# Kernel tuning notes

Hardware: AMD Instinct MI355X
Metric: run time of the kernel (lower is better)

The kernel has to match this reference:

```python
import jax, jax.numpy as jnp
import numpy as np
from jax import lax

B, C, IMG, PATCH = 128, 3, 224, 16
EMB, HEADS = 384, 6
NPATCH = (IMG // PATCH) ** 2          # 196
NTOK = NPATCH + 1                     # 197 (cls token)
HID = int(EMB * 4.0)                  # 1536 (also expert hidden)
NE, K = 4, 2                          # num_experts (hardcoded 4), top-k
NCLS = 1000


def _ln(x, g, b, eps=1e-5):
    m = jnp.mean(x, axis=-1, keepdims=True)
    v = jnp.mean((x - m) ** 2, axis=-1, keepdims=True)
    return (x - m) * lax.rsqrt(v + eps) * g + b


def setup_inputs() -> dict:
    key = jax.random.key(0)
    ks = jax.random.split(key, 16)
    s = 0.02
    return {
        "x": jax.random.normal(ks[0], (B, C, IMG, IMG), jnp.float32),
        "conv_w": jax.random.normal(ks[1], (EMB, C, PATCH, PATCH), jnp.float32) * s,
        "conv_b": jnp.zeros((EMB,), jnp.float32),
        "cls_token": jax.random.normal(ks[2], (1, 1, EMB), jnp.float32) * s,
        "pos_embed": jax.random.normal(ks[3], (1, NTOK, EMB), jnp.float32) * s,
        "ln1_g": jnp.ones((EMB,), jnp.float32),
        "ln1_b": jnp.zeros((EMB,), jnp.float32),
        "in_proj_w": jax.random.normal(ks[4], (3 * EMB, EMB), jnp.float32) * s,
        "in_proj_b": jnp.zeros((3 * EMB,), jnp.float32),
        "out_proj_w": jax.random.normal(ks[5], (EMB, EMB), jnp.float32) * s,
        "out_proj_b": jnp.zeros((EMB,), jnp.float32),
        "router_w": jax.random.normal(ks[6], (NE, EMB), jnp.float32) * s,
        "router_b": jnp.zeros((NE,), jnp.float32),
        "ew1": jax.random.normal(ks[7], (NE, EMB, HID), jnp.float32) * s,
        "eb1": jnp.zeros((NE, HID), jnp.float32),
        "ew2": jax.random.normal(ks[8], (NE, HID, EMB), jnp.float32) * s,
        "eb2": jnp.zeros((NE, EMB), jnp.float32),
        "ln2_g": jnp.ones((EMB,), jnp.float32),
        "ln2_b": jnp.zeros((EMB,), jnp.float32),
        "head_w": jax.random.normal(ks[9], (NCLS, EMB), jnp.float32) * s,
        "head_b": jnp.zeros((NCLS,), jnp.float32),
    }


def reference(x, conv_w, conv_b, cls_token, pos_embed,
              ln1_g, ln1_b, in_proj_w, in_proj_b, out_proj_w, out_proj_b,
              router_w, router_b, ew1, eb1, ew2, eb2,
              ln2_g, ln2_b, head_w, head_b):
    # ---- patch embedding: Conv2d(stride=kernel=patch) -> [B, N, E]
    h = lax.conv_general_dilated(x, conv_w, window_strides=(PATCH, PATCH),
                                 padding="VALID",
                                 dimension_numbers=("NCHW", "OIHW", "NCHW"))
    h = h + conv_b[None, :, None, None]
    h = h.reshape(B, EMB, NPATCH).transpose(0, 2, 1)          # [B, 196, E]
    h = jnp.concatenate([jnp.broadcast_to(cls_token, (B, 1, EMB)), h], axis=1)
    h = h + pos_embed                                         # [B, 197, E]

    # ---- SelfAttentionBlock (NOTE: no residual; same LN applied twice, as in source)
    hn = _ln(h, ln1_g, ln1_b)
    qkv = hn @ in_proj_w.T + in_proj_b                        # [B, N, 3E]
    q, k, v = jnp.split(qkv, 3, axis=-1)
    hd = EMB // HEADS
    q = q.reshape(B, NTOK, HEADS, hd)
    k = k.reshape(B, NTOK, HEADS, hd)
    v = v.reshape(B, NTOK, HEADS, hd)
    att = jnp.einsum("bqhd,bkhd->bhqk", q, k) / np.sqrt(hd).astype(np.float32)
    att = jax.nn.softmax(att, axis=-1)
    o = jnp.einsum("bhqk,bkhd->bqhd", att, v).reshape(B, NTOK, EMB)
    o = o @ out_proj_w.T + out_proj_b
    h = _ln(o, ln1_g, ln1_b)                                  # second LN, same params

    # ---- MoE: dense all-expert FFN + top-k gather + mean
    scores = jax.nn.softmax(h @ router_w.T + router_b, axis=-1)   # [B, N, NE]
    topk_vals, topk_idx = lax.top_k(scores, K)                    # [B, N, K]
    flat = h.reshape(B * NTOK, EMB)
    eh = jax.nn.gelu(jnp.einsum("te,neh->tnh", flat, ew1) + eb1, approximate=False)
    eo = jnp.einsum("tnh,nhe->tne", eh, ew2) + eb2                # [BN, NE, E]
    idx = topk_idx.reshape(B * NTOK, K, 1)
    sel = jnp.take_along_axis(eo, idx, axis=1)                    # [BN, K, E]
    h = sel.mean(axis=1).reshape(B, NTOK, EMB)

    # ---- final norm + classification head on cls token
    h = _ln(h, ln2_g, ln2_b)
    return h[:, 0] @ head_w.T + head_b                            # [B, NCLS]
```

## Files before the change

kernel.cpp:

```cpp
#include <hip/hip_runtime.h>
#include <cstdint>
#include <cstddef>

typedef _Float16 f16;
typedef _Float16 f16x8 __attribute__((ext_vector_type(8)));
typedef float    f32x4 __attribute__((ext_vector_type(4)));

constexpr int NTOKC  = 197;
constexpr int TTOK   = 128 * 197;
constexpr int EMB    = 384;
constexpr int HID    = 1536;

constexpr size_t OFF_CONVW  = 0;
constexpr size_t OFF_KVW    = 589824;
constexpr size_t OFF_EW1T   = 1179648;
constexpr size_t OFF_EW2T   = 5898240;
constexpr size_t OFF_OCLS   = 10616832;
constexpr size_t OFF_O2CLS  = 10813440;
constexpr size_t OFF_HCLS16 = 11010048;
constexpr size_t OFF_MASKW  = 11108352;
constexpr size_t OFF_EH     = 11110400;
constexpr size_t OFF_EO     = 12683264;
constexpr size_t OFF_H      = 13500416;
constexpr size_t OFF_XH     = 52232192;
constexpr size_t OFF_KV     = 71598080;
constexpr size_t OFF_AIM    = OFF_KV;
constexpr size_t OFF_HEADW16 = OFF_KV + (size_t)TTOK * 768 * 4;
constexpr size_t OFF_HFIN   = OFF_HEADW16 + 786432;
constexpr size_t WS_NEEDED  = OFF_HFIN + 98304;

__device__ __forceinline__ void gload16(const void* g, void* l) {
  __builtin_amdgcn_global_load_lds(
      (__attribute__((address_space(1))) void*)(void*)g,
      (__attribute__((address_space(3))) void*)l, 16, 0, 0);
}

__global__ __launch_bounds__(256) void cast_f16_k(
    const float* __restrict__ in, f16* __restrict__ o, int n) {
  int i = blockIdx.x * 256 + threadIdx.x;
  if (i < n) o[i] = (f16)in[i];
}

__global__ __launch_bounds__(256) void cast_pad_k(
    const float* __restrict__ in, f16* __restrict__ o) {
// ... 9 lines not shown
  __shared__ float tile[32][33];
  int e = blockIdx.z;
  const float* pin = in + (size_t)e * R * C;
  f16* pout = outp + (size_t)e * R * C;
  int c0 = blockIdx.x * 32, r0 = blockIdx.y * 32;
  int tx = threadIdx.x & 31, ty = threadIdx.x >> 5;
#pragma unroll
  for (int i = 0; i < 4; i++)
    tile[ty + 8 * i][tx] = pin[(size_t)(r0 + ty + 8 * i) * C + c0 + tx];
  __syncthreads();
#pragma unroll
  for (int i = 0; i < 4; i++)
    pout[(size_t)(c0 + ty + 8 * i) * R + r0 + tx] = (f16)tile[tx][ty + 8 * i];
}

__global__ void cls_init_k(const float* __restrict__ cls, const float* __restrict__ posw,
                           float* __restrict__ h0) {
  int b = blockIdx.x, c = threadIdx.x;
  h0[(size_t)b * NTOKC * EMB + c] = cls[c] + posw[c];
}

__global__ __launch_bounds__(256) void im2col_k(
    const float* __restrict__ img, f16* __restrict__ A) {
  __shared__ float tile[16 * 224];
  int py = blockIdx.x, cch = blockIdx.y, b = blockIdx.z;
  const float* src = img + ((size_t)(b * 3 + cch) * 224 + py * 16) * 224;
  for (int i = threadIdx.x; i < 16 * 224; i += 256) tile[i] = src[i];
  __syncthreads();
  if (threadIdx.x < 224) {
    int px = threadIdx.x >> 4, ky = threadIdx.x & 15;
    size_t outb = ((size_t)(b * 196 + py * 14 + px)) * 768 + cch * 256 + ky * 16;
    f16 hv[16] __attribute__((aligned(16)));
#pragma unroll
    for (int t = 0; t < 16; t++) hv[t] = (f16)tile[ky * 224 + px * 16 + t];
    ((uint4*)(A + outb))[0] = ((uint4*)hv)[0];
    ((uint4*)(A + outb))[1] = ((uint4*)hv)[1];
  }
}

template <int EMBED>
__global__ __launch_bounds__(256) void gemm16_k(
    const f16* __restrict__ A, const f16* __restrict__ B,
    const float* __restrict__ bias, const float* __restrict__ posw,
    float* __restrict__ Cout, int K, int N) {
  __shared__ f16 As[128 * 32];
  __shared__ f16 Bs[128 * 32];
  const int tid = threadIdx.x;
  const int lane = tid & 63;
  const int wave = tid >> 6;
  const int m0 = (int)blockIdx.y * 128;
  const int n0 = (int)blockIdx.x * 128;
  const int wm = (wave >> 1) * 64;
  const int wn = (wave & 1) * 64;
  const int fr = lane & 15;
  const int fq = lane >> 4;

  f32x4 acc[4][4];
#pragma unroll
  for (int i = 0; i < 4; i++)
#pragma unroll
    for (int j = 0; j < 4; j++) acc[i][j] = f32x4{0.f, 0.f, 0.f, 0.f};
// ... 21 lines not shown
    for (int i = 0; i < 4; i++)
#pragma unroll
      for (int j = 0; j < 4; j++)
        acc[i][j] = __builtin_amdgcn_mfma_f32_16x16x32_f16(af[i], bf[j], acc[i][j], 0, 0, 0);
    __syncthreads();
  }

#pragma unroll
  for (int i = 0; i < 4; i++)
#pragma unroll
    for (int j = 0; j < 4; j++)
#pragma unroll
      for (int rg = 0; rg < 4; rg++) {
        int gm = m0 + wm + i * 16 + fq * 4 + rg;
        int gn = n0 + wn + j * 16 + fr;
        float v = acc[i][j][rg] + bias[gn];
        if (EMBED) {
          int bb = gm / 196;
          int pp = gm - bb * 196;
          Cout[((size_t)bb * NTOKC + pp + 1) * EMB + gn] =
              v + posw[(size_t)(pp + 1) * EMB + gn];
        } else {
          Cout[(size_t)gm * N + gn] = v;
        }
      }
}

template <int GELU>
__global__ __launch_bounds__(256) void moe_gemm_k(
    const f16* __restrict__ A, size_t aestride,
    const f16* __restrict__ Bm, size_t bestride,
    const float* __restrict__ bias, int biasstride,
    f16* __restrict__ outh, float* __restrict__ outf, size_t ostride,
    int K, int N) {
  __shared__ f16 As[128 * 32];
  __shared__ f16 Bs[128 * 32];
  const int tid = threadIdx.x;
  const int lane = tid & 63;
  const int wave = tid >> 6;
  const int e = (int)blockIdx.y;
  const int n0 = (int)blockIdx.x * 128;
  const int wm = (wave >> 1) * 64;
  const int wn = (wave & 1) * 64;
  const int fr = lane & 15;
  const int fq = lane >> 4;
  A += (size_t)e * aestride;
  Bm += (size_t)e * bestride;
  bias += (size_t)e * biasstride;

  f32x4 acc[4][4];
#pragma unroll
  for (int i = 0; i < 4; i++)
#pragma unroll
    for (int j = 0; j < 4; j++) acc[i][j] = f32x4{0.f, 0.f, 0.f, 0.f};

  const int srow = wave * 32 + (lane >> 2);
  const int scol = (lane & 3) * 8;
  const f16* ag = A + (size_t)srow * K + scol;
  const f16* bg = Bm + (size_t)(n0 + srow) * K + scol;
  const size_t rstep = (size_t)16 * K;
  f16* la = As + wave * 32 * 32;
  f16* lb = Bs + wave * 32 * 32;

  for (int k0 = 0; k0 < K; k0 += 32) {
    gload16(ag, la);          gload16(ag + rstep, la + 16 * 32);
    gload16(bg, lb);          gload16(bg + rstep, lb + 16 * 32);
    ag += 32; bg += 32;
    __syncthreads();
    f16x8 af[4], bf[4];
#pragma unroll
    for (int i = 0; i < 4; i++) {
      af[i] = *(const f16x8*)&As[(wm + i * 16 + fr) * 32 + fq * 8];
      bf[i] = *(const f16x8*)&Bs[(wn + i * 16 + fr) * 32 + fq * 8];
    }
#pragma unroll
    for (int i = 0; i < 4; i++)
#pragma unroll
      for (int j = 0; j < 4; j++)
        acc[i][j] = __builtin_amdgcn_mfma_f32_16x16x32_f16(af[i], bf[j], acc[i][j], 0, 0, 0);
    __syncthreads();
  }

#pragma unroll
  for (int i = 0; i < 4; i++)
#pragma unroll
    for (int j = 0; j < 4; j++)
#pragma unroll
      for (int rg = 0; rg < 4; rg++) {
        int gm = wm + i * 16 + fq * 4 + rg;
        int gn = n0 + wn + j * 16 + fr;
        float v = acc[i][j][rg] + bias[gn];
        if (GELU) {
          float g = 0.5f * v * (1.0f + erff(v * 0.70710678118654752f));
          outh[(size_t)e * ostride + (size_t)gm * N + gn] = (f16)g;
        } else {
          outf[(size_t)e * ostride + (size_t)gm * N + gn] = v;
        }
      }
}

__global__ __launch_bounds__(256) void head_gemm_k(
    const f16* __restrict__ A, const f16* __restrict__ B,
    const float* __restrict__ hb, float* __restrict__ outp) {
  __shared__ f16 As[128 * 32];
  __shared__ f16 Bs[128 * 32];
  const int K = 384;
  const int tid = threadIdx.x;
  const int lane = tid & 63;
  const int wave = tid >> 6;
  const int n0 = (int)blockIdx.x * 128;
  const int wm = (wave >> 1) * 64;
  const int wn = (wave & 1) * 64;
  const int fr = lane & 15;
// ... 31 lines not shown
        acc[i][j] = __builtin_amdgcn_mfma_f32_16x16x32_f16(af[i], bf[j], acc[i][j], 0, 0, 0);
    __syncthreads();
  }

#pragma unroll
  for (int i = 0; i < 4; i++)
#pragma unroll
    for (int j = 0; j < 4; j++)
#pragma unroll
      for (int rg = 0; rg < 4; rg++) {
        int gm = wm + i * 16 + fq * 4 + rg;
        int gn = n0 + wn + j * 16 + fr;
        if (gn < 1000)
          outp[(size_t)gm * 1000 + gn] = acc[i][j][rg] + hb[gn];
      }
}

__global__ __launch_bounds__(256) void ln_k(
    const float* __restrict__ in, const float* __restrict__ g, const float* __restrict__ bb,
    f16* __restrict__ oh) {
  int wave = threadIdx.x >> 6, lane = threadIdx.x & 63;
  size_t row = (size_t)blockIdx.x * 4 + wave;
  const float* xp = in + row * EMB;
  float v[6];
  float s = 0.f, sq = 0.f;
#pragma unroll
  for (int i = 0; i < 6; i++) {
    v[i] = xp[lane + 64 * i];
    s += v[i];
    sq += v[i] * v[i];
  }
#pragma unroll
  for (int off = 32; off; off >>= 1) {
    s += __shfl_xor(s, off);
    sq += __shfl_xor(sq, off);
  }
  float m = s * (1.f / 384.f);
  float var = sq * (1.f / 384.f) - m * m;
  float rs = rsqrtf(var + 1e-5f);
#pragma unroll
  for (int i = 0; i < 6; i++) {
    int c = lane + 64 * i;
    oh[row * EMB + c] = (f16)((v[i] - m) * rs * g[c] + bb[c]);
  }
}

__global__ __launch_bounds__(256) void attn_cls_k(
    const float* __restrict__ Hbuf, const float* __restrict__ g, const float* __restrict__ bb,
    const float* __restrict__ Wq, const float* __restrict__ bq,
    const float* __restrict__ kv, float* __restrict__ ocls) {
  __shared__ float xs[EMB];
  __shared__ float qs[64];
  __shared__ float red[8];
  __shared__ float qpart[4][64];
  __shared__ float racc[64 * 64];
  __shared__ float rsum[64];
  const int h = blockIdx.x, b = blockIdx.y;
  const int tid = threadIdx.x;
  const int wave = tid >> 6, lane = tid & 63;

  const float* xp = Hbuf + (size_t)b * NTOKC * EMB;
  float v0 = xp[tid];
  float v1 = (tid < 128) ? xp[256 + tid] : 0.f;
  float s = v0 + v1, sq = v0 * v0 + v1 * v1;
#pragma unroll
  for (int off = 32; off; off >>= 1) {
    s += __shfl_xor(s, off);
    sq += __shfl_xor(sq, off);
  }
  if (lane == 0) { red[wave] = s; red[4 + wave] = sq; }
  __syncthreads();
  float S = red[0] + red[1] + red[2] + red[3];
  float SQ = red[4] + red[5] + red[6] + red[7];
  float m = S * (1.f / 384.f);
  float rs = rsqrtf(SQ * (1.f / 384.f) - m * m + 1e-5f);
  xs[tid] = (v0 - m) * rs * g[tid] + bb[tid];
  if (tid < 128) xs[256 + tid] = (v1 - m) * rs * g[256 + tid] + bb[256 + tid];
  __syncthreads();

  {
    int d = tid & 63, part = tid >> 6;
    const float4* w4 = (const float4*)(Wq + (size_t)(h * 64 + d) * EMB + part * 96);
    const float4* s4 = (const float4*)(xs + part * 96);
    float a = 0.f;
#pragma unroll
    for (int i = 0; i < 24; i++) {
      float4 xx = s4[i], ww = w4[i];
      a += xx.x * ww.x + xx.y * ww.y + xx.z * ww.z + xx.w * ww.w;
    }
    qpart[part][d] = a;
  }
  __syncthreads();
  if (tid < 64)
    qs[tid] = bq[h * 64 + tid] + qpart[0][tid] + qpart[1][tid] + qpart[2][tid] + qpart[3][tid];
  __syncthreads();

  const int r4 = lane >> 2, c = lane & 3;
  const int rowslot = wave * 16 + r4;
  float qv[16];
#pragma unroll
  for (int j = 0; j < 16; j++) qv[j] = qs[c * 16 + j];
  float acc[16];
#pragma unroll
  for (int j = 0; j < 16; j++) acc[j] = 0.f;
  float lsum = 0.f;

#pragma unroll
  for (int i = 0; i < 4; i++) {
    int row = rowslot + 64 * i;
    if (row < NTOKC) {
      const float4* kp = (const float4*)(kv + ((size_t)b * NTOKC + row) * 768 + h * 64 + c * 16);
      float4 k0 = kp[0], k1 = kp[1], k2 = kp[2], k3 = kp[3];
      float sc = qv[0] * k0.x + qv[1] * k0.y + qv[2] * k0.z + qv[3] * k0.w +
                 qv[4] * k1.x + qv[5] * k1.y + qv[6] * k1.z + qv[7] * k1.w +
                 qv[8] * k2.x + qv[9] * k2.y + qv[10] * k2.z + qv[11] * k2.w +
                 qv[12] * k3.x + qv[13] * k3.y + qv[14] * k3.z + qv[15] * k3.w;
      sc += __shfl_xor(sc, 1);
      sc += __shfl_xor(sc, 2);
      float p = __expf(sc * 0.125f);
      lsum += p;
      const float4* vp = (const float4*)(kv + ((size_t)b * NTOKC + row) * 768 + 384 + h * 64 + c * 16);
      float4 w0 = vp[0], w1 = vp[1], w2 = vp[2], w3 = vp[3];
      acc[0] += p * w0.x;  acc[1] += p * w0.y;  acc[2] += p * w0.z;  acc[3] += p * w0.w;
      acc[4] += p * w1.x;  acc[5] += p * w1.y;  acc[6] += p * w1.z;  acc[7] += p * w1.w;
      acc[8] += p * w2.x;  acc[9] += p * w2.y;  acc[10] += p * w2.z; acc[11] += p * w2.w;
      acc[12] += p * w3.x; acc[13] += p * w3.y; acc[14] += p * w3.z; acc[15] += p * w3.w;
    }
  }
#pragma unroll
  for (int j = 0; j < 16; j++) racc[rowslot * 64 + c * 16 + j] = acc[j];
  if (c == 0) rsum[rowslot] = lsum;
  __syncthreads();

  if (tid < 64) {
    float o = 0.f, ls = 0.f;
#pragma unroll 8
    for (int r = 0; r < 64; r++) {
      o += racc[r * 64 + tid];
      ls += rsum[r];
    }
    ocls[(size_t)b * EMB + h * 64 + tid] = o / ls;
  }
}

__global__ __launch_bounds__(384) void rowproj_k(
    const float* __restrict__ xf, const float* __restrict__ W,
    const float* __restrict__ bias, float* __restrict__ outp) {
  __shared__ float hx[EMB];
  int b = blockIdx.x, t = threadIdx.x;
  hx[t] = xf[(size_t)b * EMB + t];
  __syncthreads();
  const float4* w4 = (const float4*)(W + (size_t)t * EMB);
  const float4* s4 = (const float4*)hx;
  float a = bias[t];
#pragma unroll 8
  for (int i = 0; i < 96; i++) {
    float4 x = s4[i], w = w4[i];
    a += x.x * w.x + x.y * w.y + x.z * w.z + x.w * w.w;
  }
  outp[(size_t)b * EMB + t] = a;
}

__global__ __launch_bounds__(384) void ln_router_k(
    const float* __restrict__ o2cls, const float* __restrict__ g, const float* __restrict__ bb,
    const float* __restrict__ rw, const float* __restrict__ rb,
    f16* __restrict__ hcls16, float* __restrict__ maskw) {
  __shared__ float red[16];
  __shared__ float part[6][4];
  __shared__ float logits[4];
  int b = blockIdx.x, t = threadIdx.x;
  int lane = t & 63, wave = t >> 6;
  float v = o2cls[(size_t)b * EMB + t];
  float s = v, sq = v * v;
#pragma unroll
  for (int off = 32; off; off >>= 1) {
    s += __shfl_xor(s, off);
    sq += __shfl_xor(sq, off);
  }
  if (lane == 0) { red[wave] = s; red[8 + wave] = sq; }
  __syncthreads();
  float S = 0.f, SQ = 0.f;
#pragma unroll
  for (int i = 0; i < 6; i++) { S += red[i]; SQ += red[8 + i]; }
  float m = S * (1.f / 384.f);
  float rs = rsqrtf(SQ * (1.f / 384.f) - m * m + 1e-5f);
  float y = (v - m) * rs * g[t] + bb[t];
  hcls16[(size_t)b * EMB + t] = (f16)y;
  float p0 = y * rw[t];
  float p1 = y * rw[EMB + t];
  float p2 = y * rw[2 * EMB + t];
  float p3 = y * rw[3 * EMB + t];
#pragma unroll
  for (int off = 32; off; off >>= 1) {
    p0 += __shfl_xor(p0, off);
    p1 += __shfl_xor(p1, off);
    p2 += __shfl_xor(p2, off);
    p3 += __shfl_xor(p3, off);
  }
  if (lane == 0) { part[wave][0] = p0; part[wave][1] = p1; part[wave][2] = p2; part[wave][3] = p3; }
  __syncthreads();
  if (t < 4) {
    float a = rb[t];
#pragma unroll
    for (int i = 0; i < 6; i++) a += part[i][t];
    logits[t] = a;
  }
  __syncthreads();
  if (t == 0) {
    float l0 = logits[0], l1 = logits[1], l2 = logits[2], l3 = logits[3];
    int i1 = 0; float b1 = l0;
    if (l1 > b1) { b1 = l1; i1 = 1; }
    if (l2 > b1) { b1 = l2; i1 = 2; }
    if (l3 > b1) { b1 = l3; i1 = 3; }
    int i2 = -1; float b2 = 0.f;
    float lv[4] = {l0, l1, l2, l3};
#pragma unroll
    for (int i = 0; i < 4; i++) {
      if (i == i1) continue;
      if (i2 < 0 || lv[i] > b2) { i2 = i; b2 = lv[i]; }
    }
#pragma unroll
    for (int e = 0; e < 4; e++)
      maskw[(size_t)b * 4 + e] = (e == i1 || e == i2) ? 0.5f : 0.f;
  }
}

__global__ __launch_bounds__(384) void combine_ln2_k(
    const float* __restrict__ eo, const float* __restrict__ maskw,
    const float* __restrict__ g, const float* __restrict__ bb,
    f16* __restrict__ hfin) {
  __shared__ float red[16];
  int b = blockIdx.x, t = threadIdx.x;
  int lane = t & 63, wave = t >> 6;
  float mw0 = maskw[b * 4 + 0], mw1 = maskw[b * 4 + 1];
  float mw2 = maskw[b * 4 + 2], mw3 = maskw[b * 4 + 3];
  const size_t eb = (size_t)b * EMB;
  const size_t es = (size_t)128 * EMB;
  float v = mw0 * eo[eb + t] + mw1 * eo[es + eb + t] +
            mw2 * eo[2 * es + eb + t] + mw3 * eo[3 * es + eb + t];
  float s = v, sq = v * v;
#pragma unroll
  for (int off = 32; off; off >>= 1) {
    s += __shfl_xor(s, off);
    sq += __shfl_xor(sq, off);
  }
  if (lane == 0) { red[wave] = s; red[8 + wave] = sq; }
  __syncthreads();
  float S = 0.f, SQ = 0.f;
#pragma unroll
  for (int i = 0; i < 6; i++) { S += red[i]; SQ += red[8 + i]; }
  float m = S * (1.f / 384.f);
  float rs = rsqrtf(SQ * (1.f / 384.f) - m * m + 1e-5f);
  hfin[(size_t)b * EMB + t] = (f16)((v - m) * rs * g[t] + bb[t]);
}

extern "C" void kernel_launch(void* const* d_in, const int* in_sizes, int n_in,
                              void* d_out, int out_size, void* d_ws, size_t ws_size,
                              hipStream_t stream) {
  const float* x      = (const float*)d_in[0];
  const float* conv_w = (const float*)d_in[1];
  const float* conv_b = (const float*)d_in[2];
  const float* cls_t  = (const float*)d_in[3];
  const float* pos    = (const float*)d_in[4];
  const float* ln1_g  = (const float*)d_in[5];
  const float* ln1_b  = (const float*)d_in[6];
  const float* inp_w  = (const float*)d_in[7];
  const float* inp_b  = (const float*)d_in[8];
  const float* outp_w = (const float*)d_in[9];
// ... 4 lines not shown
  const float* eb1    = (const float*)d_in[14];
  const float* ew2    = (const float*)d_in[15];
  const float* eb2    = (const float*)d_in[16];
  const float* ln2_g  = (const float*)d_in[17];
  const float* ln2_b  = (const float*)d_in[18];
  const float* head_w = (const float*)d_in[19];
  const float* head_b = (const float*)d_in[20];
  float* out = (float*)d_out;
  char* w = (char*)d_ws;
  if (ws_size < WS_NEEDED) return;

  f16* convw    = (f16*)(w + OFF_CONVW);
  f16* kvw      = (f16*)(w + OFF_KVW);
  f16* ew1t     = (f16*)(w + OFF_EW1T);
  f16* ew2t     = (f16*)(w + OFF_EW2T);
  float* ocls   = (float*)(w + OFF_OCLS);
  float* o2cls  = (float*)(w + OFF_O2CLS);
  f16* hcls16   = (f16*)(w + OFF_HCLS16);
  float* maskw  = (float*)(w + OFF_MASKW);
  f16* ehbuf    = (f16*)(w + OFF_EH);
  float* eobuf  = (float*)(w + OFF_EO);
  float* Hbuf   = (float*)(w + OFF_H);
  f16* xh       = (f16*)(w + OFF_XH);
  float* kvbuf  = (float*)(w + OFF_KV);
  f16* aim      = (f16*)(w + OFF_AIM);
  f16* headw16  = (f16*)(w + OFF_HEADW16);
  f16* hfin     = (f16*)(w + OFF_HFIN);

  cast_f16_k<<<dim3((294912 + 255) / 256), 256, 0, stream>>>(conv_w, convw, 294912);
  cast_f16_k<<<dim3((294912 + 255) / 256), 256, 0, stream>>>(inp_w + 384 * 384, kvw, 294912);
  cast_pad_k<<<dim3((1024 * 384 + 255) / 256), 256, 0, stream>>>(head_w, headw16);
  transpose_cast_k<<<dim3(48, 12, 4), 256, 0, stream>>>(ew1, ew1t, 384, 1536);
  transpose_cast_k<<<dim3(12, 48, 4), 256, 0, stream>>>(ew2, ew2t, 1536, 384);

  im2col_k<<<dim3(14, 3, 128), 256, 0, stream>>>(x, aim);
  gemm16_k<1><<<dim3(3, 196), 256, 0, stream>>>(aim, convw, conv_b, pos, Hbuf, 768, EMB);
  cls_init_k<<<dim3(128), dim3(384), 0, stream>>>(cls_t, pos, Hbuf);

  ln_k<<<dim3(TTOK / 4), 256, 0, stream>>>(Hbuf, ln1_g, ln1_b, xh);

  gemm16_k<0><<<dim3(6, 197), 256, 0, stream>>>(xh, kvw, inp_b + 384, nullptr, kvbuf, EMB, 768);

  attn_cls_k<<<dim3(6, 128), 256, 0, stream>>>(
      Hbuf, ln1_g, ln1_b, inp_w, inp_b, kvbuf, ocls);

  rowproj_k<<<dim3(128), 384, 0, stream>>>(ocls, outp_w, outp_b, o2cls);

  ln_router_k<<<dim3(128), 384, 0, stream>>>(
      o2cls, ln1_g, ln1_b, rt_w, rt_b, hcls16, maskw);

  moe_gemm_k<1><<<dim3(12, 4), 256, 0, stream>>>(
      hcls16, 0, ew1t, (size_t)HID * EMB, eb1, HID,
      ehbuf, nullptr, (size_t)128 * HID, EMB, HID);
  moe_gemm_k<0><<<dim3(3, 4), 256, 0, stream>>>(
      ehbuf, (size_t)128 * HID, ew2t, (size_t)EMB * HID, eb2, EMB,
      nullptr, eobuf, (size_t)128 * EMB, HID, EMB);

  combine_ln2_k<<<dim3(128), 384, 0, stream>>>(eobuf, maskw, ln2_g, ln2_b, hfin);
  head_gemm_k<<<dim3(8), 256, 0, stream>>>(hfin, headw16, head_b, out);
  (void)in_sizes; (void)n_in; (void)out_size;
}
```

Before: 394.5 us.

## Fuse patch-embed GEMM with LayerNorm, store K/V in fp16, split-K the MoE GEMMs

Replaces the patch-embedding GEMM plus separate LayerNorm pass with one kernel. It computes full 384-wide rows per block and applies bias, positional embedding and LN in registers, writing fp16 activations directly. This removes the fp32 H buffer round trip. The cls-token LN and Q projection are computed once in a single block and broadcast, since the cls input is the same across the batch. K/V are stored as fp16 to halve attention read traffic. The MoE GEMMs get smaller N tiles and split-K partials to raise block counts, at the cost of an extra partial-sum reduction in the combine kernel and reduced KV precision.

```diff
diff --git a/kernel.cpp b/kernel.cpp
--- a/kernel.cpp
+++ b/kernel.cpp
@@ -11,23 +11,24 @@
 constexpr int EMB    = 384;
 constexpr int HID    = 1536;
 
-constexpr size_t OFF_CONVW  = 0;
-constexpr size_t OFF_KVW    = 589824;
-constexpr size_t OFF_EW1T   = 1179648;
-constexpr size_t OFF_EW2T   = 5898240;
-constexpr size_t OFF_OCLS   = 10616832;
-constexpr size_t OFF_O2CLS  = 10813440;
-constexpr size_t OFF_HCLS16 = 11010048;
-constexpr size_t OFF_MASKW  = 11108352;
-constexpr size_t OFF_EH     = 11110400;
-constexpr size_t OFF_EO     = 12683264;
-constexpr size_t OFF_H      = 13500416;
-constexpr size_t OFF_XH     = 52232192;
-constexpr size_t OFF_KV     = 71598080;
-constexpr size_t OFF_AIM    = OFF_KV;
-constexpr size_t OFF_HEADW16 = OFF_KV + (size_t)TTOK * 768 * 4;
-constexpr size_t OFF_HFIN   = OFF_HEADW16 + 786432;
-constexpr size_t WS_NEEDED  = OFF_HFIN + 98304;
+constexpr size_t OFF_CONVW   = 0;
+constexpr size_t OFF_KVW     = 589824;
+constexpr size_t OFF_EW1T    = 1179648;
+constexpr size_t OFF_EW2T    = 5898240;
+constexpr size_t OFF_HEADW16 = 10616832;
+constexpr size_t OFF_XCLS16  = 11403264;
+constexpr size_t OFF_Q       = 11404800;
+constexpr size_t OFF_OCLS    = 11406336;
+constexpr size_t OFF_O2CLS   = 11602944;
+constexpr size_t OFF_HCLS16  = 11799552;
+constexpr size_t OFF_MASKW   = 11897856;
+constexpr size_t OFF_EH      = 11899904;
+constexpr size_t OFF_EPART   = 13472768;
+constexpr size_t OFF_HFIN    = 16618496;
+constexpr size_t OFF_XH      = 16716800;
+constexpr size_t OFF_KV      = 36082688;
+constexpr size_t OFF_AIM     = 74814464;
+constexpr size_t WS_NEEDED   = 113349632;
 
 __device__ __forceinline__ void gload16(const void* g, void* l) {
   __builtin_amdgcn_global_load_lds(
@@ -67,10 +68,47 @@
     pout[(size_t)(c0 + ty + 8 * i) * R + r0 + tx] = (f16)tile[tx][ty + 8 * i];
 }
 
-__global__ void cls_init_k(const float* __restrict__ cls, const float* __restrict__ posw,
-                           float* __restrict__ h0) {
-  int b = blockIdx.x, c = threadIdx.x;
-  h0[(size_t)b * NTOKC * EMB + c] = cls[c] + posw[c];
+__global__ __launch_bounds__(384) void clsprep_k(
+    const float* __restrict__ cls, const float* __restrict__ posw,
+    const float* __restrict__ g, const float* __restrict__ bb,
+    const float* __restrict__ Wq, const float* __restrict__ bq,
+    f16* __restrict__ xcls16, float* __restrict__ qout) {
+  __shared__ float xs[EMB];
+  __shared__ float red[16];
+  int t = threadIdx.x, lane = t & 63, wave = t >> 6;
+  float v = cls[t] + posw[t];
+  float s = v, sq = v * v;
+#pragma unroll
+  for (int off = 32; off; off >>= 1) {
+    s += __shfl_xor(s, off);
+    sq += __shfl_xor(sq, off);
+  }
+  if (lane == 0) { red[wave] = s; red[8 + wave] = sq; }
+  __syncthreads();
+  float S = 0.f, SQ = 0.f;
+#pragma unroll
+  for (int i = 0; i < 6; i++) { S += red[i]; SQ += red[8 + i]; }
+  float m = S * (1.f / 384.f);
+  float rs = rsqrtf(SQ * (1.f / 384.f) - m * m + 1e-5f);
+  float y = (v - m) * rs * g[t] + bb[t];
+  xs[t] = y;
+  xcls16[t] = (f16)y;
+  __syncthreads();
+  const float4* w4 = (const float4*)(Wq + (size_t)t * EMB);
+  const float4* s4 = (const float4*)xs;
+  float a = bq[t];
+#pragma unroll 8
+  for (int i = 0; i < 96; i++) {
+    float4 xx = s4[i], ww = w4[i];
+    a += xx.x * ww.x + xx.y * ww.y + xx.z * ww.z + xx.w * ww.w;
+  }
+  qout[t] = a;
+}
+
+__global__ __launch_bounds__(384) void bcast_cls_k(
+    const f16* __restrict__ xcls16, f16* __restrict__ xh) {
+  int b = blockIdx.x, t = threadIdx.x;
+  xh[(size_t)b * NTOKC * EMB + t] = xcls16[t];
 }
 
 __global__ __launch_bounds__(256) void im2col_k(
@@ -91,13 +129,92 @@
   }
 }
 
-template <int EMBED>
-__global__ __launch_bounds__(256) void gemm16_k(
+__global__ __launch_bounds__(256) void embed_ln_k(
     const f16* __restrict__ A, const f16* __restrict__ B,
     const float* __restrict__ bias, const float* __restrict__ posw,
-    float* __restrict__ Cout, int K, int N) {
+    const float* __restrict__ g, const float* __restrict__ bb,
+    f16* __restrict__ xh) {
+  __shared__ f16 As[64 * 32];
+  __shared__ f16 Bs[384 * 32];
+  const int K = 768;
+  const int tid = threadIdx.x;
+  const int lane = tid & 63;
+  const int wave = tid >> 6;
+  const int m0 = (int)blockIdx.x * 64;
+  const int fr = lane & 15;
+  const int fq = lane >> 4;
+
+  f32x4 acc[24];
+#pragma unroll
+  for (int j = 0; j < 24; j++) acc[j] = f32x4{0.f, 0.f, 0.f, 0.f};
+
+  const int sr = lane >> 2;
+  const int sc = (lane & 3) * 8;
+  const f16* ag = A + (size_t)(m0 + wave * 16 + sr) * K + sc;
+  f16* la = As + wave * 16 * 32;
+  const f16* bg = B + (size_t)(wave * 96 + sr) * K + sc;
+  f16* lb = Bs + wave * 96 * 32;
+
+  for (int k0 = 0; k0 < K; k0 += 32) {
+    gload16(ag + k0, la);
+#pragma unroll
+    for (int t = 0; t < 6; t++)
+      gload16(bg + (size_t)(t * 16) * K + k0, lb + t * 16 * 32);
+    __syncthreads();
+    f16x8 af = *(const f16x8*)&As[(wave * 16 + fr) * 32 + fq * 8];
+#pragma unroll
+    for (int j = 0; j < 24; j++) {
+      f16x8 bf = *(const f16x8*)&Bs[(j * 16 + fr) * 32 + fq * 8];
+      acc[j] = __builtin_amdgcn_mfma_f32_16x16x32_f16(af, bf, acc[j], 0, 0, 0);
+    }
+    __syncthreads();
+  }
+
+  float* sCB = (float*)Bs;
+  float* sG  = sCB + 384;
+  float* sB2 = sG + 384;
+  for (int i = tid; i < 384; i += 256) {
+    sCB[i] = bias[i]; sG[i] = g[i]; sB2[i] = bb[i];
+  }
+  __syncthreads();
+
+#pragma unroll
+  for (int rg = 0; rg < 4; rg++) {
+    int row = m0 + wave * 16 + fq * 4 + rg;
+    int bimg = row / 196;
+    int pp = row - bimg * 196;
+    const float* prow = posw + (size_t)(pp + 1) * EMB;
+    float v[24];
+    float s = 0.f, sq = 0.f;
+#pragma unroll
+    for (int j = 0; j < 24; j++) {
+      int col = j * 16 + fr;
+      float t = acc[j][rg] + sCB[col] + prow[col];
+      v[j] = t;
+      s += t; sq += t * t;
+    }
+#pragma unroll
+    for (int off = 1; off < 16; off <<= 1) {
+      s += __shfl_xor(s, off);
+      sq += __shfl_xor(sq, off);
+    }
+    float m = s * (1.f / 384.f);
+    float rs = rsqrtf(sq * (1.f / 384.f) - m * m + 1e-5f);
+    f16* orow = xh + ((size_t)bimg * NTOKC + pp + 1) * EMB;
+#pragma unroll
+    for (int j = 0; j < 24; j++) {
+      int col = j * 16 + fr;
+      orow[col] = (f16)((v[j] - m) * rs * sG[col] + sB2[col]);
+    }
+  }
+}
+
+__global__ __launch_bounds__(256) void gemm_kv_k(
+    const f16* __restrict__ A, const f16* __restrict__ B,
+    const float* __restrict__ bias, f16* __restrict__ Cout) {
   __shared__ f16 As[128 * 32];
   __shared__ f16 Bs[128 * 32];
+  const int K = EMB, N = 768;
   const int tid = threadIdx.x;
   const int lane = tid & 63;
   const int wave = tid >> 6;
@@ -149,69 +266,200 @@
       for (int rg = 0; rg < 4; rg++) {
         int gm = m0 + wm + i * 16 + fq * 4 + rg;
         int gn = n0 + wn + j * 16 + fr;
-        float v = acc[i][j][rg] + bias[gn];
-        if (EMBED) {
-          int bb = gm / 196;
-          int pp = gm - bb * 196;
-          Cout[((size_t)bb * NTOKC + pp + 1) * EMB + gn] =
-              v + posw[(size_t)(pp + 1) * EMB + gn];
-        } else {
-          Cout[(size_t)gm * N + gn] = v;
-        }
+        Cout[(size_t)gm * N + gn] = (f16)(acc[i][j][rg] + bias[gn]);
       }
 }
 
-template <int GELU>
-__global__ __launch_bounds__(256) void moe_gemm_k(
-    const f16* __restrict__ A, size_t aestride,
-    const f16* __restrict__ Bm, size_t bestride,
-    const float* __restrict__ bias, int biasstride,
-    f16* __restrict__ outh, float* __restrict__ outf, size_t ostride,
-    int K, int N) {
+__global__ __launch_bounds__(256) void attn_cls_k(
+    const float* __restrict__ qg, const f16* __restrict__ kv,
+    float* __restrict__ ocls) {
+  __shared__ float racc[64 * 64];
+  __shared__ float rsum[64];
+  const int h = blockIdx.x, b = blockIdx.y;
+  const int tid = threadIdx.x;
+  const int wave = tid >> 6, lane = tid & 63;
+  const int r4 = lane >> 2, c = lane & 3;
+  const int rowslot = wave * 16 + r4;
+
+  float qv[16];
+#pragma unroll
+  for (int j = 0; j < 16; j++) qv[j] = qg[h * 64 + c * 16 + j];
+  float acc[16];
+#pragma unroll
+  for (int j = 0; j < 16; j++) acc[j] = 0.f;
+  float lsum = 0.f;
+
+#pragma unroll
+  for (int i = 0; i < 4; i++) {
+    int row = rowslot + 64 * i;
+    if (row < NTOKC) {
+      const f16* kp = kv + ((size_t)b * NTOKC + row) * 768 + h * 64 + c * 16;
+      f16x8 k0 = *(const f16x8*)kp;
+      f16x8 k1 = *(const f16x8*)(kp + 8);
+      float sc = 0.f;
+#pragma unroll
+      for (int j = 0; j < 8; j++) sc += qv[j] * (float)k0[j];
+#pragma unroll
+      for (int j = 0; j < 8; j++) sc += qv[8 + j] * (float)k1[j];
+      sc += __shfl_xor(sc, 1);
+      sc += __shfl_xor(sc, 2);
+      float p = __expf(sc * 0.125f);
+      lsum += p;
+      const f16* vp = kp + 384;
+      f16x8 v0 = *(const f16x8*)vp;
+      f16x8 v1 = *(const f16x8*)(vp + 8);
+#pragma unroll
+      for (int j = 0; j < 8; j++) acc[j] += p * (float)v0[j];
+#pragma unroll
+      for (int j = 0; j < 8; j++) acc[8 + j] += p * (float)v1[j];
+    }
+  }
+#pragma unroll
+  for (int j = 0; j < 16; j++) racc[rowslot * 64 + c * 16 + j] = acc[j];
+  if (c == 0) rsum[rowslot] = lsum;
+  __syncthreads();
+
+  if (tid < 64) {
+    float o = 0.f, ls = 0.f;
+#pragma unroll 8
+    for (int r = 0; r < 64; r++) {
+      o += racc[r * 64 + tid];
+      ls += rsum[r];
+    }
+    ocls[(size_t)b * EMB + h * 64 + tid] = o / ls;
+  }
+}
+
+__global__ __launch_bounds__(384) void rowproj_k(
+    const float* __restrict__ xf, const float* __restrict__ W,
+    const float* __restrict__ bias, float* __restrict__ outp) {
+  __shared__ float hx[EMB];
+  int b = blockIdx.x, t = threadIdx.x;
+  hx[t] = xf[(size_t)b * EMB + t];
+  __syncthreads();
+  const float4* w4 = (const float4*)(W + (size_t)t * EMB);
+  const float4* s4 = (const float4*)hx;
+  float a = bias[t];
+#pragma unroll 8
+  for (int i = 0; i < 96; i++) {
+    float4 x = s4[i], w = w4[i];
+    a += x.x * w.x + x.y * w.y + x.z * w.z + x.w * w.w;
+  }
+  outp[(size_t)b * EMB + t] = a;
+}
+
+__global__ __launch_bounds__(384) void ln_router_k(
+    const float* __restrict__ o2cls, const float* __restrict__ g, const float* __restrict__ bb,
+    const float* __restrict__ rw, const float* __restrict__ rb,
+    f16* __restrict__ hcls16, float* __restrict__ maskw) {
+  __shared__ float red[16];
+  __shared__ float part[6][4];
+  __shared__ float logits[4];
+  int b = blockIdx.x, t = threadIdx.x;
+  int lane = t & 63, wave = t >> 6;
+  float v = o2cls[(size_t)b * EMB + t];
+  float s = v, sq = v * v;
+#pragma unroll
+  for (int off = 32; off; off >>= 1) {
+    s += __shfl_xor(s, off);
+    sq += __shfl_xor(sq, off);
+  }
+  if (lane == 0) { red[wave] = s; red[8 + wave] = sq; }
+  __syncthreads();
+  float S = 0.f, SQ = 0.f;
+#pragma unroll
+  for (int i = 0; i < 6; i++) { S += red[i]; SQ += red[8 + i]; }
+  float m = S * (1.f / 384.f);
+  float rs = rsqrtf(SQ * (1.f / 384.f) - m * m + 1e-5f);
+  float y = (v - m) * rs * g[t] + bb[t];
+  hcls16[(size_t)b * EMB + t] = (f16)y;
+  float p0 = y * rw[t];
+  float p1 = y * rw[EMB + t];
+  float p2 = y * rw[2 * EMB + t];
+  float p3 = y * rw[3 * EMB + t];
+#pragma unroll
+  for (int off = 32; off; off >>= 1) {
+    p0 += __shfl_xor(p0, off);
+    p1 += __shfl_xor(p1, off);
+    p2 += __shfl_xor(p2, off);
+    p3 += __shfl_xor(p3, off);
+  }
+  if (lane == 0) { part[wave][0] = p0; part[wave][1] = p1; part[wave][2] = p2; part[wave][3] = p3; }
+  __syncthreads();
+  if (t < 4) {
+    float a = rb[t];
+#pragma unroll
+    for (int i = 0; i < 6; i++) a += part[i][t];
+    logits[t] = a;
+  }
+  __syncthreads();
+  if (t == 0) {
+    float l0 = logits[0], l1 = logits[1], l2 = logits[2], l3 = logits[3];
+    int i1 = 0; float b1 = l0;
+    if (l1 > b1) { b1 = l1; i1 = 1; }
+    if (l2 > b1) { b1 = l2; i1 = 2; }
+    if (l3 > b1) { b1 = l3; i1 = 3; }
+    int i2 = -1; float b2 = 0.f;
+    float lv[4] = {l0, l1, l2, l3};
+#pragma unroll
+    for (int i = 0; i < 4; i++) {
+      if (i == i1) continue;
+      if (i2 < 0 || lv[i] > b2) { i2 = i; b2 = lv[i]; }
+    }
+#pragma unroll
+    for (int e = 0; e < 4; e++)
+      maskw[(size_t)b * 4 + e] = (e == i1 || e == i2) ? 0.5f : 0.f;
+  }
+}
+
+__global__ __launch_bounds__(256) void moe1_k(
+    const f16* __restrict__ A, const f16* __restrict__ Bm,
+    const float* __restrict__ bias, f16* __restrict__ outh) {
   __shared__ f16 As[128 * 32];
-  __shared__ f16 Bs[128 * 32];
+  __shared__ f16 Bs[64 * 32];
+  const int K = EMB;
   const int tid = threadIdx.x;
   const int lane = tid & 63;
   const int wave = tid >> 6;
   const int e = (int)blockIdx.y;
-  const int n0 = (int)blockIdx.x * 128;
+  const int n0 = (int)blockIdx.x * 64;
   const int wm = (wave >> 1) * 64;
-  const int wn = (wave & 1) * 64;
+  const int wn = (wave & 1) * 32;
   const int fr = lane & 15;
   const int fq = lane >> 4;
-  A += (size_t)e * aestride;
-  Bm += (size_t)e * bestride;
-  bias += (size_t)e * biasstride;
-
-  f32x4 acc[4][4];
-#pragma unroll
-  for (int i = 0; i < 4; i++)
-#pragma unroll
-    for (int j = 0; j < 4; j++) acc[i][j] = f32x4{0.f, 0.f, 0.f, 0.f};
-
-  const int srow = wave * 32 + (lane >> 2);
-  const int scol = (lane & 3) * 8;
-  const f16* ag = A + (size_t)srow * K + scol;
-  const f16* bg = Bm + (size_t)(n0 + srow) * K + scol;
+  Bm += (size_t)e * HID * EMB;
+  bias += (size_t)e * HID;
+
+  f32x4 acc[4][2];
+#pragma unroll
+  for (int i = 0; i < 4; i++)
+#pragma unroll
+    for (int j = 0; j < 2; j++) acc[i][j] = f32x4{0.f, 0.f, 0.f, 0.f};
+
+  const int sr = lane >> 2;
+  const int sc = (lane & 3) * 8;
+  const f16* ag = A + (size_t)(wave * 32 + sr) * K + sc;
+  const f16* bg = Bm + (size_t)(n0 + wave * 16 + sr) * K + sc;
   const size_t rstep = (size_t)16 * K;
   f16* la = As + wave * 32 * 32;
-  f16* lb = Bs + wave * 32 * 32;
+  f16* lb = Bs + wave * 16 * 32;
 
   for (int k0 = 0; k0 < K; k0 += 32) {
-    gload16(ag, la);          gload16(ag + rstep, la + 16 * 32);
-    gload16(bg, lb);          gload16(bg + rstep, lb + 16 * 32);
+    gload16(ag, la);  gload16(ag + rstep, la + 16 * 32);
+    gload16(bg, lb);
     ag += 32; bg += 32;
     __syncthreads();
-    f16x8 af[4], bf[4];
-#pragma unroll
-    for (int i = 0; i < 4; i++) {
+    f16x8 af[4], bf[2];
+#pragma unroll
+    for (int i = 0; i < 4; i++)
       af[i] = *(const f16x8*)&As[(wm + i * 16 + fr) * 32 + fq * 8];
-      bf[i] = *(const f16x8*)&Bs[(wn + i * 16 + fr) * 32 + fq * 8];
-    }
+#pragma unroll
+    for (int j = 0; j < 2; j++)
+      bf[j] = *(const f16x8*)&Bs[(wn + j * 16 + fr) * 32 + fq * 8];
 #pragma unroll
     for (int i = 0; i < 4; i++)
 #pragma unroll
-      for (int j = 0; j < 4; j++)
+      for (int j = 0; j < 2; j++)
         acc[i][j] = __builtin_amdgcn_mfma_f32_16x16x32_f16(af[i], bf[j], acc[i][j], 0, 0, 0);
     __syncthreads();
   }
@@ -219,19 +467,112 @@
 #pragma unroll
   for (int i = 0; i < 4; i++)
 #pragma unroll
-    for (int j = 0; j < 4; j++)
+    for (int j = 0; j < 2; j++)
 #pragma unroll
       for (int rg = 0; rg < 4; rg++) {
         int gm = wm + i * 16 + fq * 4 + rg;
         int gn = n0 + wn + j * 16 + fr;
         float v = acc[i][j][rg] + bias[gn];
-        if (GELU) {
-          float g = 0.5f * v * (1.0f + erff(v * 0.70710678118654752f));
-          outh[(size_t)e * ostride + (size_t)gm * N + gn] = (f16)g;
-        } else {
-          outf[(size_t)e * ostride + (size_t)gm * N + gn] = v;
-        }
+        float gl = 0.5f * v * (1.0f + erff(v * 0.70710678118654752f));
+        outh[(size_t)e * 128 * HID + (size_t)gm * HID + gn] = (f16)gl;
       }
+}
+
+__global__ __launch_bounds__(256) void moe2_k(
+    const f16* __restrict__ EH, const f16* __restrict__ W2,
+    float* __restrict__ part) {
+  __shared__ f16 As[128 * 32];
+  __shared__ f16 Bs[64 * 32];
+  const int tid = threadIdx.x;
+  const int lane = tid & 63;
+  const int wave = tid >> 6;
+  const int n0 = (int)blockIdx.x * 64;
+  const int e = (int)blockIdx.y;
+  const int kc = (int)blockIdx.z;
+  const int wm = (wave >> 1) * 64;
+  const int wn = (wave & 1) * 32;
+  const int fr = lane & 15;
+  const int fq = lane >> 4;
+  const f16* A = EH + (size_t)e * 128 * HID + kc * 384;
+  const f16* B = W2 + (size_t)e * EMB * HID + kc * 384;
+
+  f32x4 acc[4][2];
+#pragma unroll
+  for (int i = 0; i < 4; i++)
+#pragma unroll
+    for (int j = 0; j < 2; j++) acc[i][j] = f32x4{0.f, 0.f, 0.f, 0.f};
+
+  const int sr = lane >> 2;
+  const int sc = (lane & 3) * 8;
+  const f16* ag = A + (size_t)(wave * 32 + sr) * HID + sc;
+  const f16* bg = B + (size_t)(n0 + wave * 16 + sr) * HID + sc;
+  const size_t rstep = (size_t)16 * HID;
+  f16* la = As + wave * 32 * 32;
+  f16* lb = Bs + wave * 16 * 32;
+
+  for (int k0 = 0; k0 < 384; k0 += 32) {
+    gload16(ag, la);  gload16(ag + rstep, la + 16 * 32);
+    gload16(bg, lb);
+    ag += 32; bg += 32;
+    __syncthreads();
+    f16x8 af[4], bf[2];
+#pragma unroll
+    for (int i = 0; i < 4; i++)
+      af[i] = *(const f16x8*)&As[(wm + i * 16 + fr) * 32 + fq * 8];
+#pragma unroll
+    for (int j = 0; j < 2; j++)
+      bf[j] = *(const f16x8*)&Bs[(wn + j * 16 + fr) * 32 + fq * 8];
+#pragma unroll
+    for (int i = 0; i < 4; i++)
+#pragma unroll
+      for (int j = 0; j < 2; j++)
+        acc[i][j] = __builtin_amdgcn_mfma_f32_16x16x32_f16(af[i], bf[j], acc[i][j], 0, 0, 0);
+    __syncthreads();
+  }
+
+#pragma unroll
+  for (int i = 0; i < 4; i++)
+#pragma unroll
+    for (int j = 0; j < 2; j++)
+#pragma unroll
+      for (int rg = 0; rg < 4; rg++) {
+        int gm = wm + i * 16 + fq * 4 + rg;
+        int gn = n0 + wn + j * 16 + fr;
+        part[(((size_t)kc * 4 + e) * 128 + gm) * EMB + gn] = acc[i][j][rg];
+      }
+}
+
+__global__ __launch_bounds__(384) void combine_ln2_k(
+    const float* __restrict__ part, const float* __restrict__ eb2,
+    const float* __restrict__ maskw,
+    const float* __restrict__ g, const float* __restrict__ bb,
+    f16* __restrict__ hfin) {
+  __shared__ float red[16];
+  int b = blockIdx.x, t = threadIdx.x;
+  int lane = t & 63, wave = t >> 6;
+  float v = 0.f;
+#pragma unroll
+  for (int e = 0; e < 4; e++) {
+    float s = eb2[e * EMB + t];
+#pragma unroll
+    for (int kc = 0; kc < 4; kc++)
+      s += part[(((size_t)kc * 4 + e) * 128 + b) * EMB + t];
+    v += maskw[b * 4 + e] * s;
+  }
+  float s = v, sq = v * v;
+#pragma unroll
+  for (int off = 32; off; off >>= 1) {
+    s += __shfl_xor(s, off);
+    sq += __shfl_xor(sq, off);
+  }
+  if (lane == 0) { red[wave] = s; red[8 + wave] = sq; }
+  __syncthreads();
+  float S = 0.f, SQ = 0.f;
+#pragma unroll
+  for (int i = 0; i < 6; i++) { S += red[i]; SQ += red[8 + i]; }
+  float m = S * (1.f / 384.f);
+  float rs = rsqrtf(SQ * (1.f / 384.f) - m * m + 1e-5f);
+  hfin[(size_t)b * EMB + t] = (f16)((v - m) * rs * g[t] + bb[t]);
 }
 
 __global__ __launch_bounds__(256) void head_gemm_k(
@@ -293,244 +634,6 @@
         if (gn < 1000)
           outp[(size_t)gm * 1000 + gn] = acc[i][j][rg] + hb[gn];
       }
-}
-
-__global__ __launch_bounds__(256) void ln_k(
-    const float* __restrict__ in, const float* __restrict__ g, const float* __restrict__ bb,
-    f16* __restrict__ oh) {
-  int wave = threadIdx.x >> 6, lane = threadIdx.x & 63;
-  size_t row = (size_t)blockIdx.x * 4 + wave;
-  const float* xp = in + row * EMB;
-  float v[6];
-  float s = 0.f, sq = 0.f;
-#pragma unroll
-  for (int i = 0; i < 6; i++) {
-    v[i] = xp[lane + 64 * i];
-    s += v[i];
-    sq += v[i] * v[i];
-  }
-#pragma unroll
-  for (int off = 32; off; off >>= 1) {
-    s += __shfl_xor(s, off);
-    sq += __shfl_xor(sq, off);
-  }
-  float m = s * (1.f / 384.f);
-  float var = sq * (1.f / 384.f) - m * m;
-  float rs = rsqrtf(var + 1e-5f);
-#pragma unroll
-  for (int i = 0; i < 6; i++) {
-    int c = lane + 64 * i;
-    oh[row * EMB + c] = (f16)((v[i] - m) * rs * g[c] + bb[c]);
-  }
-}
-
-__global__ __launch_bounds__(256) void attn_cls_k(
-    const float* __restrict__ Hbuf, const float* __restrict__ g, const float* __restrict__ bb,
-    const float* __restrict__ Wq, const float* __restrict__ bq,
-    const float* __restrict__ kv, float* __restrict__ ocls) {
-  __shared__ float xs[EMB];
-  __shared__ float qs[64];
-  __shared__ float red[8];
-  __shared__ float qpart[4][64];
-  __shared__ float racc[64 * 64];
-  __shared__ float rsum[64];
-  const int h = blockIdx.x, b = blockIdx.y;
-  const int tid = threadIdx.x;
-  const int wave = tid >> 6, lane = tid & 63;
-
-  const float* xp = Hbuf + (size_t)b * NTOKC * EMB;
-  float v0 = xp[tid];
-  float v1 = (tid < 128) ? xp[256 + tid] : 0.f;
-  float s = v0 + v1, sq = v0 * v0 + v1 * v1;
-#pragma unroll
-  for (int off = 32; off; off >>= 1) {
-    s += __shfl_xor(s, off);
-    sq += __shfl_xor(sq, off);
-  }
-  if (lane == 0) { red[wave] = s; red[4 + wave] = sq; }
-  __syncthreads();
-  float S = red[0] + red[1] + red[2] + red[3];
-  float SQ = red[4] + red[5] + red[6] + red[7];
-  float m = S * (1.f / 384.f);
-  float rs = rsqrtf(SQ * (1.f / 384.f) - m * m + 1e-5f);
-  xs[tid] = (v0 - m) * rs * g[tid] + bb[tid];
-  if (tid < 128) xs[256 + tid] = (v1 - m) * rs * g[256 + tid] + bb[256 + tid];
-  __syncthreads();
-
-  {
-    int d = tid & 63, part = tid >> 6;
-    const float4* w4 = (const float4*)(Wq + (size_t)(h * 64 + d) * EMB + part * 96);
-    const float4* s4 = (const float4*)(xs + part * 96);
-    float a = 0.f;
-#pragma unroll
-    for (int i = 0; i < 24; i++) {
-      float4 xx = s4[i], ww = w4[i];
-      a += xx.x * ww.x + xx.y * ww.y + xx.z * ww.z + xx.w * ww.w;
-    }
-    qpart[part][d] = a;
-  }
-  __syncthreads();
-  if (tid < 64)
-    qs[tid] = bq[h * 64 + tid] + qpart[0][tid] + qpart[1][tid] + qpart[2][tid] + qpart[3][tid];
-  __syncthreads();
-
-  const int r4 = lane >> 2, c = lane & 3;
-  const int rowslot = wave * 16 + r4;
-  float qv[16];
-#pragma unroll
-  for (int j = 0; j < 16; j++) qv[j] = qs[c * 16 + j];
-  float acc[16];
-#pragma unroll
-  for (int j = 0; j < 16; j++) acc[j] = 0.f;
-  float lsum = 0.f;
-
-#pragma unroll
-  for (int i = 0; i < 4; i++) {
-    int row = rowslot + 64 * i;
-    if (row < NTOKC) {
-      const float4* kp = (const float4*)(kv + ((size_t)b * NTOKC + row) * 768 + h * 64 + c * 16);
-      float4 k0 = kp[0], k1 = kp[1], k2 = kp[2], k3 = kp[3];
-      float sc = qv[0] * k0.x + qv[1] * k0.y + qv[2] * k0.z + qv[3] * k0.w +
-                 qv[4] * k1.x + qv[5] * k1.y + qv[6] * k1.z + qv[7] * k1.w +
-                 qv[8] * k2.x + qv[9] * k2.y + qv[10] * k2.z + qv[11] * k2.w +
-                 qv[12] * k3.x + qv[13] * k3.y + qv[14] * k3.z + qv[15] * k3.w;
-      sc += __shfl_xor(sc, 1);
-      sc += __shfl_xor(sc, 2);
-      float p = __expf(sc * 0.125f);
-      lsum += p;
-      const float4* vp = (const float4*)(kv + ((size_t)b * NTOKC + row) * 768 + 384 + h * 64 + c * 16);
-      float4 w0 = vp[0], w1 = vp[1], w2 = vp[2], w3 = vp[3];
-      acc[0] += p * w0.x;  acc[1] += p * w0.y;  acc[2] += p * w0.z;  acc[3] += p * w0.w;
-      acc[4] += p * w1.x;  acc[5] += p * w1.y;  acc[6] += p * w1.z;  acc[7] += p * w1.w;
-      acc[8] += p * w2.x;  acc[9] += p * w2.y;  acc[10] += p * w2.z; acc[11] += p * w2.w;
-      acc[12] += p * w3.x; acc[13] += p * w3.y; acc[14] += p * w3.z; acc[15] += p * w3.w;
-    }
-  }
-#pragma unroll
-  for (int j = 0; j < 16; j++) racc[rowslot * 64 + c * 16 + j] = acc[j];
-  if (c == 0) rsum[rowslot] = lsum;
-  __syncthreads();
-
-  if (tid < 64) {
-    float o = 0.f, ls = 0.f;
-#pragma unroll 8
-    for (int r = 0; r < 64; r++) {
-      o += racc[r * 64 + tid];
-      ls += rsum[r];
-    }
-    ocls[(size_t)b * EMB + h * 64 + tid] = o / ls;
-  }
-}
-
-__global__ __launch_bounds__(384) void rowproj_k(
-    const float* __restrict__ xf, const float* __restrict__ W,
-    const float* __restrict__ bias, float* __restrict__ outp) {
-  __shared__ float hx[EMB];
-  int b = blockIdx.x, t = threadIdx.x;
-  hx[t] = xf[(size_t)b * EMB + t];
-  __syncthreads();
-  const float4* w4 = (const float4*)(W + (size_t)t * EMB);
-  const float4* s4 = (const float4*)hx;
-  float a = bias[t];
-#pragma unroll 8
-  for (int i = 0; i < 96; i++) {
-    float4 x = s4[i], w = w4[i];
-    a += x.x * w.x + x.y * w.y + x.z * w.z + x.w * w.w;
-  }
-  outp[(size_t)b * EMB + t] = a;
-}
-
-__global__ __launch_bounds__(384) void ln_router_k(
-    const float* __restrict__ o2cls, const float* __restrict__ g, const float* __restrict__ bb,
-    const float* __restrict__ rw, const float* __restrict__ rb,
-    f16* __restrict__ hcls16, float* __restrict__ maskw) {
-  __shared__ float red[16];
-  __shared__ float part[6][4];
-  __shared__ float logits[4];
-  int b = blockIdx.x, t = threadIdx.x;
-  int lane = t & 63, wave = t >> 6;
-  float v = o2cls[(size_t)b * EMB + t];
-  float s = v, sq = v * v;
-#pragma unroll
-  for (int off = 32; off; off >>= 1) {
-    s += __shfl_xor(s, off);
-    sq += __shfl_xor(sq, off);
-  }
-  if (lane == 0) { red[wave] = s; red[8 + wave] = sq; }
-  __syncthreads();
-  float S = 0.f, SQ = 0.f;
-#pragma unroll
-  for (int i = 0; i < 6; i++) { S += red[i]; SQ += red[8 + i]; }
-  float m = S * (1.f / 384.f);
-  float rs = rsqrtf(SQ * (1.f / 384.f) - m * m + 1e-5f);
-  float y = (v - m) * rs * g[t] + bb[t];
-  hcls16[(size_t)b * EMB + t] = (f16)y;
-  float p0 = y * rw[t];
-  float p1 = y * rw[EMB + t];
-  float p2 = y * rw[2 * EMB + t];
-  float p3 = y * rw[3 * EMB + t];
-#pragma unroll
-  for (int off = 32; off; off >>= 1) {
-    p0 += __shfl_xor(p0, off);
-    p1 += __shfl_xor(p1, off);
-    p2 += __shfl_xor(p2, off);
-    p3 += __shfl_xor(p3, off);
-  }
-  if (lane == 0) { part[wave][0] = p0; part[wave][1] = p1; part[wave][2] = p2; part[wave][3] = p3; }
-  __syncthreads();
-  if (t < 4) {
-    float a = rb[t];
-#pragma unroll
-    for (int i = 0; i < 6; i++) a += part[i][t];
-    logits[t] = a;
-  }
-  __syncthreads();
-  if (t == 0) {
-    float l0 = logits[0], l1 = logits[1], l2 = logits[2], l3 = logits[3];
-    int i1 = 0; float b1 = l0;
-    if (l1 > b1) { b1 = l1; i1 = 1; }
-    if (l2 > b1) { b1 = l2; i1 = 2; }
-    if (l3 > b1) { b1 = l3; i1 = 3; }
-    int i2 = -1; float b2 = 0.f;
-    float lv[4] = {l0, l1, l2, l3};
-#pragma unroll
-    for (int i = 0; i < 4; i++) {
-      if (i == i1) continue;
-      if (i2 < 0 || lv[i] > b2) { i2 = i; b2 = lv[i]; }
-    }
-#pragma unroll
-    for (int e = 0; e < 4; e++)
-      maskw[(size_t)b * 4 + e] = (e == i1 || e == i2) ? 0.5f : 0.f;
-  }
-}
-
-__global__ __launch_bounds__(384) void combine_ln2_k(
-    const float* __restrict__ eo, const float* __restrict__ maskw,
-    const float* __restrict__ g, const float* __restrict__ bb,
-    f16* __restrict__ hfin) {
-  __shared__ float red[16];
-  int b = blockIdx.x, t = threadIdx.x;
-  int lane = t & 63, wave = t >> 6;
-  float mw0 = maskw[b * 4 + 0], mw1 = maskw[b * 4 + 1];
-  float mw2 = maskw[b * 4 + 2], mw3 = maskw[b * 4 + 3];
-  const size_t eb = (size_t)b * EMB;
-  const size_t es = (size_t)128 * EMB;
-  float v = mw0 * eo[eb + t] + mw1 * eo[es + eb + t] +
-            mw2 * eo[2 * es + eb + t] + mw3 * eo[3 * es + eb + t];
-  float s = v, sq = v * v;
-#pragma unroll
-  for (int off = 32; off; off >>= 1) {
-    s += __shfl_xor(s, off);
-    sq += __shfl_xor(sq, off);
-  }
-  if (lane == 0) { red[wave] = s; red[8 + wave] = sq; }
-  __syncthreads();
-  float S = 0.f, SQ = 0.f;
-#pragma unroll
-  for (int i = 0; i < 6; i++) { S += red[i]; SQ += red[8 + i]; }
-  float m = S * (1.f / 384.f);
-  float rs = rsqrtf(SQ * (1.f / 384.f) - m * m + 1e-5f);
-  hfin[(size_t)b * EMB + t] = (f16)((v - m) * rs * g[t] + bb[t]);
 }
 
 extern "C" void kernel_launch(void* const* d_in, const int* in_sizes, int n_in,
@@ -565,18 +668,19 @@
   f16* kvw      = (f16*)(w + OFF_KVW);
   f16* ew1t     = (f16*)(w + OFF_EW1T);
   f16* ew2t     = (f16*)(w + OFF_EW2T);
+  f16* headw16  = (f16*)(w + OFF_HEADW16);
+  f16* xcls16   = (f16*)(w + OFF_XCLS16);
+  float* qvec   = (float*)(w + OFF_Q);
   float* ocls   = (float*)(w + OFF_OCLS);
   float* o2cls  = (float*)(w + OFF_O2CLS);
   f16* hcls16   = (f16*)(w + OFF_HCLS16);
   float* maskw  = (float*)(w + OFF_MASKW);
   f16* ehbuf    = (f16*)(w + OFF_EH);
-  float* eobuf  = (float*)(w + OFF_EO);
-  float* Hbuf   = (float*)(w + OFF_H);
+  float* epart  = (float*)(w + OFF_EPART);
+  f16* hfin     = (f16*)(w + OFF_HFIN);
   f16* xh       = (f16*)(w + OFF_XH);
-  float* kvbuf  = (float*)(w + OFF_KV);
+  f16* kvbuf    = (f16*)(w + OFF_KV);
   f16* aim      = (f16*)(w + OFF_AIM);
-  f16* headw16  = (f16*)(w + OFF_HEADW16);
-  f16* hfin     = (f16*)(w + OFF_HFIN);
 
   cast_f16_k<<<dim3((294912 + 255) / 256), 256, 0, stream>>>(conv_w, convw, 294912);
   cast_f16_k<<<dim3((294912 + 255) / 256), 256, 0, stream>>>(inp_w + 384 * 384, kvw, 294912);
@@ -584,30 +688,25 @@
   transpose_cast_k<<<dim3(48, 12, 4), 256, 0, stream>>>(ew1, ew1t, 384, 1536);
   transpose_cast_k<<<dim3(12, 48, 4), 256, 0, stream>>>(ew2, ew2t, 1536, 384);
 
+  clsprep_k<<<dim3(1), 384, 0, stream>>>(cls_t, pos, ln1_g, ln1_b, inp_w, inp_b, xcls16, qvec);
+  bcast_cls_k<<<dim3(128), 384, 0, stream>>>(xcls16, xh);
+
   im2col_k<<<dim3(14, 3, 128), 256, 0, stream>>>(x, aim);
-  gemm16_k<1><<<dim3(3, 196), 256, 0, stream>>>(aim, convw, conv_b, pos, Hbuf, 768, EMB);
-  cls_init_k<<<dim3(128), dim3(384), 0, stream>>>(cls_t, pos, Hbuf);
-
-  ln_k<<<dim3(TTOK / 4), 256, 0, stream>>>(Hbuf, ln1_g, ln1_b, xh);
-
-  gemm16_k<0><<<dim3(6, 197), 256, 0, stream>>>(xh, kvw, inp_b + 384, nullptr, kvbuf, EMB, 768);
-
-  attn_cls_k<<<dim3(6, 128), 256, 0, stream>>>(
-      Hbuf, ln1_g, ln1_b, inp_w, inp_b, kvbuf, ocls);
+  embed_ln_k<<<dim3(392), 256, 0, stream>>>(aim, convw, conv_b, pos, ln1_g, ln1_b, xh);
+
+  gemm_kv_k<<<dim3(6, 197), 256, 0, stream>>>(xh, kvw, inp_b + 384, kvbuf);
+
+  attn_cls_k<<<dim3(6, 128), 256, 0, stream>>>(qvec, kvbuf, ocls);
 
   rowproj_k<<<dim3(128), 384, 0, stream>>>(ocls, outp_w, outp_b, o2cls);
 
   ln_router_k<<<dim3(128), 384, 0, stream>>>(
       o2cls, ln1_g, ln1_b, rt_w, rt_b, hcls16, maskw);
 
-  moe_gemm_k<1><<<dim3(12, 4), 256, 0, stream>>>(
-      hcls16, 0, ew1t, (size_t)HID * EMB, eb1, HID,
-      ehbuf, nullptr, (size_t)128 * HID, EMB, HID);
-  moe_gemm_k<0><<<dim3(3, 4), 256, 0, stream>>>(
-      ehbuf, (size_t)128 * HID, ew2t, (size_t)EMB * HID, eb2, EMB,
-      nullptr, eobuf, (size_t)128 * EMB, HID, EMB);
-
-  combine_ln2_k<<<dim3(128), 384, 0, stream>>>(eobuf, maskw, ln2_g, ln2_b, hfin);
+  moe1_k<<<dim3(24, 4), 256, 0, stream>>>(hcls16, ew1t, eb1, ehbuf);
+  moe2_k<<<dim3(6, 4, 4), 256, 0, stream>>>(ehbuf, ew2t, epart);
+  combine_ln2_k<<<dim3(128), 384, 0, stream>>>(epart, eb2, maskw, ln2_g, ln2_b, hfin);
+
   head_gemm_k<<<dim3(8), 256, 0, stream>>>(hfin, headw16, head_b, out);
   (void)in_sizes; (void)n_in; (void)out_size;
 }
```

New measurement: 377.1 us. 4.4% less time.
